# Performance work log

Hardware: AMD Instinct MI355X
Metric: run time of the kernel (lower is better)

## Reference

```python
import jax, jax.numpy as jnp
import numpy as np

BN_EPS = 1e-5
R = 8.0        # radius
L = 11         # sequence kernel size (odd), s = L//2
K = 24         # kernel_channels[-1]
N_NODES = 32768
N_EDGES = 524288
C_IN = 128     # in_channels == out_channels
C_W = 32       # width = out_channels * base_width / 64


def _bn(x, gamma, beta):
    # BatchNorm1d in training mode: biased batch statistics over node dim
    mu = jnp.mean(x, axis=0)
    var = jnp.mean(jnp.square(x - mu), axis=0)
    return (x - mu) * jax.lax.rsqrt(var + BN_EPS) * gamma + beta


def _lrelu(x, slope):
    return jnp.where(x >= 0, x, slope * x)


def setup_inputs() -> dict:
    key = jax.random.key(0)
    ks = jax.random.split(key, 10)

    def glorot(k, shape, fan_in):
        return jax.random.normal(k, shape, jnp.float32) * np.float32(1.0 / np.sqrt(fan_in))

    inp = {}
    inp["x"] = jax.random.normal(ks[0], (N_NODES, C_IN), jnp.float32)
    inp["pos"] = jax.random.normal(ks[1], (N_NODES, 3), jnp.float32) * 10.0
    inp["ori"] = jax.random.normal(ks[2], (N_NODES, 9), jnp.float32)
    inp["seq"] = jnp.arange(N_NODES, dtype=jnp.int32)
    inp["edge_index"] = jax.random.randint(ks[3], (2, N_EDGES), 0, N_NODES, jnp.int32)
    # input MLP params: BN(C_IN) -> LeakyReLU(0.1) -> Linear(C_IN->C_W, no bias) -> BN(C_W) -> LeakyReLU(0.1)
    inp["bn1_g"] = jnp.ones((C_IN,), jnp.float32)
    inp["bn1_b"] = jnp.zeros((C_IN,), jnp.float32)
    inp["lin1_w"] = glorot(ks[4], (C_IN, C_W), C_IN)
    inp["bn2_g"] = jnp.ones((C_W,), jnp.float32)
    inp["bn2_b"] = jnp.zeros((C_W,), jnp.float32)
    # CDConv WeightNet (single layer kernel_channels=[K]): per-seq-bin affine 7 -> K
    inp["wn_w"] = glorot(ks[5], (L, 7, K), 7)
    inp["wn_b"] = jnp.zeros((L, K), jnp.float32)
    # CDConv output projection: [K*C_W, C_W]
    inp["conv_w"] = glorot(ks[6], (K * C_W, C_W), K * C_W)
    # output Linear: BN(C_W) -> LeakyReLU(0.1) -> Linear(C_W->C_IN, no bias)
    inp["bn3_g"] = jnp.ones((C_W,), jnp.float32)
    inp["bn3_b"] = jnp.zeros((C_W,), jnp.float32)
    inp["lin2_w"] = glorot(ks[7], (C_W, C_IN), C_W)
    return inp


def reference(x, pos, ori, seq, edge_index,
              bn1_g, bn1_b, lin1_w, bn2_g, bn2_b,
              wn_w, wn_b, conv_w, bn3_g, bn3_b, lin2_w):
    n = x.shape[0]
    identity = x  # in_channels == out_channels -> identity branch is passthrough

    # ----- input MLP (mid_channels=None) -----
    h = _lrelu(_bn(x, bn1_g, bn1_b), 0.1)
    h = h @ lin1_w                       # [N, C_W]
    h = _lrelu(_bn(h, bn2_g, bn2_b), 0.1)

    # ----- CDConv: continuous geometric kernel over neighbor edges -----
    src, dst = edge_index[0], edge_index[1]      # message j=src -> i=dst
    d = pos[src] - pos[dst]                      # [E,3]
    dist = jnp.linalg.norm(d, axis=-1, keepdims=True)
    direction = d / (dist + 1e-9)
    Ri = ori[dst].reshape(-1, 3, 3)              # receiver local frame
    Rj = ori[src].reshape(-1, 3, 3)
    pos_local = jnp.einsum('eij,ej->ei', Ri, direction)      # direction in local frame
    ori_feat = jnp.einsum('eij,ej->ei', Ri, Rj[:, 0, :])     # neighbor axis in local frame
    delta = jnp.concatenate([pos_local, ori_feat, dist / R], axis=-1)  # [E,7]

    s = L // 2
    sidx = jnp.clip(seq[src] - seq[dst], -s, s) + s          # [E] in [0, L)

    # WeightNet: per-edge affine selected by sequence bin, LeakyReLU(0.2)
    w = _lrelu(jnp.einsum('ef,efk->ek', delta, wn_w[sidx]) + wn_b[sidx], 0.2)  # [E,K]

    # message = outer(kernel_weight, x_j), scatter-sum to receivers
    msg = (w[:, :, None] * h[src][:, None, :]).reshape(w.shape[0], K * C_W)   # [E, K*C_W]
    agg = jax.ops.segment_sum(msg, dst, num_segments=n)                        # [N, K*C_W]
    h = agg @ conv_w                                                            # [N, C_W]

    # ----- output Linear + residual -----
    h = _lrelu(_bn(h, bn3_g, bn3_b), 0.1)
    out = h @ lin2_w + identity
    return out
```

## Files before the change

kernel.cpp:

```cpp
#include <hip/hip_runtime.h>

#define N_NODES 32768
#define C_IN 128
#define C_W 32
#define KK 24
#define SS 5
#define GG 8

__global__ void __launch_bounds__(256) k_pre(
        const float* __restrict__ x, float* __restrict__ s1,
        const int* __restrict__ ei, int E, int* __restrict__ counts) {
    int t = threadIdx.x;
    int c = t % C_IN;
    int r0 = blockIdx.x * 2 + t / C_IN;
    float s = 0.f, sq = 0.f;
    for (int r = r0; r < N_NODES; r += 512) {
        float v = x[(size_t)r * C_IN + c];
        s += v; sq += v * v;
    }
    atomicAdd(&s1[c], s);
    atomicAdd(&s1[C_IN + c], sq);
    for (int e = blockIdx.x * 256 + t; e < E; e += 256 * 256)
        atomicAdd(&counts[ei[E + e]], 1);
}

__global__ void __launch_bounds__(256) k_mlp1(
        const float* __restrict__ x, const float* __restrict__ s1,
        const float* __restrict__ g1, const float* __restrict__ b1,
        const float* __restrict__ w1, float* __restrict__ hpre,
        float* __restrict__ s2sh) {
    __shared__ float sAB[2][C_IN];
    __shared__ float sx[32][C_IN + 4];
    __shared__ float sw[C_IN][C_W];
    const int t = threadIdx.x;
    const int row0 = blockIdx.x * 32;
    if (t < C_IN) {
        float mean = s1[t] * (1.f / N_NODES);
        float var = s1[C_IN + t] * (1.f / N_NODES) - mean * mean;
        float a = g1[t] * rsqrtf(var + 1e-5f);
        sAB[0][t] = a; sAB[1][t] = b1[t] - mean * a;
    }
    for (int idx = t; idx < C_IN * C_W; idx += 256)
        sw[idx / C_W][idx % C_W] = w1[idx];
    __syncthreads();
    for (int idx = t; idx < 32 * 32; idx += 256) {
        int r = idx >> 5, cq = idx & 31;
        float4 v = *(const float4*)&x[(size_t)(row0 + r) * C_IN + cq * 4];
        float* d = &sx[r][cq * 4];
        float a0 = sAB[0][cq*4+0]*v.x + sAB[1][cq*4+0];
        float a1 = sAB[0][cq*4+1]*v.y + sAB[1][cq*4+1];
        float a2 = sAB[0][cq*4+2]*v.z + sAB[1][cq*4+2];
        float a3 = sAB[0][cq*4+3]*v.w + sAB[1][cq*4+3];
        d[0] = a0 >= 0.f ? a0 : 0.1f * a0;
        d[1] = a1 >= 0.f ? a1 : 0.1f * a1;
        d[2] = a2 >= 0.f ? a2 : 0.1f * a2;
        d[3] = a3 >= 0.f ? a3 : 0.1f * a3;
    }
    __syncthreads();
    const int r = t >> 3, c0 = (t & 7) * 4;
    float ac0 = 0.f, ac1 = 0.f, ac2 = 0.f, ac3 = 0.f;
    #pragma unroll 8
    for (int cc = 0; cc < C_IN; ++cc) {
        float xv = sx[r][cc];
        float4 wv = *(const float4*)&sw[cc][c0];
        ac0 += xv * wv.x; ac1 += xv * wv.y; ac2 += xv * wv.z; ac3 += xv * wv.w;
    }
    float4 o; o.x = ac0; o.y = ac1; o.z = ac2; o.w = ac3;
    *(float4*)&hpre[(size_t)(row0 + r) * C_W + c0] = o;
    __syncthreads();
    sx[r][c0] = ac0; sx[r][c0+1] = ac1; sx[r][c0+2] = ac2; sx[r][c0+3] = ac3;
    __syncthreads();
    if (t < C_W) {
        float s = 0.f, sq = 0.f;
        #pragma unroll
        for (int rr = 0; rr < 32; ++rr) {
            float v = sx[rr][t];
            s += v; sq += v * v;
        }
        int sh = (blockIdx.x & 7) * 64;
        atomicAdd(&s2sh[sh + t], s);
        atomicAdd(&s2sh[sh + C_W + t], sq);
    }
}

__global__ void __launch_bounds__(1024) k_scan1(
        const int* __restrict__ counts, int* __restrict__ scanned,
        int* __restrict__ blockSums) {
    __shared__ int s[1024];
    int t = threadIdx.x;
    int i = blockIdx.x * 1024 + t;
    int v = counts[i];
    s[t] = v;
    __syncthreads();
    for (int d = 1; d < 1024; d <<= 1) {
        int u = (t >= d) ? s[t - d] : 0;
        __syncthreads();
        s[t] += u;
        __syncthreads();
    }
    scanned[i] = s[t] - v;
    if (t == 1023) blockSums[blockIdx.x] = s[1023];
}

__global__ void k_scan2(int* __restrict__ blockSums, int* __restrict__ blockOff,
                        int* __restrict__ offsets) {
    __shared__ int s[32];
    int t = threadIdx.x;
    int v = blockSums[t];
    s[t] = v;
    __syncthreads();
    for (int d = 1; d < 32; d <<= 1) {
        int u = (t >= d) ? s[t - d] : 0;
        __syncthreads();
        s[t] += u;
        __syncthreads();
    }
    blockOff[t] = s[t] - v;
    if (t == 31) offsets[N_NODES] = s[31];
}

__global__ void __launch_bounds__(1024) k_scan3(
        const int* __restrict__ scanned, const int* __restrict__ blockOff,
        int* __restrict__ offsets, int* __restrict__ cursor) {
    int t = threadIdx.x;
    int i = blockIdx.x * 1024 + t;
    int v = scanned[i] + blockOff[blockIdx.x];
    offsets[i] = v;
    cursor[i] = v;
}

__global__ void __launch_bounds__(256) k_edge(
        const int* __restrict__ ei, int E,
        const float* __restrict__ pos, const float* __restrict__ ori,
        const int* __restrict__ seq,
        const float* __restrict__ wnw, const float* __restrict__ wnb,
        int* __restrict__ cursor, int* __restrict__ srcPerm,
        float* __restrict__ wPerm) {
    __shared__ float sWnw[11][169];
    __shared__ float sWnb[11][24];
    const int t = threadIdx.x;
    for (int idx = t; idx < 11 * 168; idx += 256)
        sWnw[idx / 168][idx % 168] = wnw[idx];
    for (int idx = t; idx < 11 * 24; idx += 256)
        sWnb[idx / 24][idx % 24] = wnb[idx];
    __syncthreads();
    const int e = blockIdx.x * 256 + t;
    if (e >= E) return;
    const int src = ei[e];
    const int dst = ei[E + e];
    int ds = seq[src] - seq[dst];
    ds = ds < -SS ? -SS : (ds > SS ? SS : ds);
    const int sb = ds + SS;
    float dx = pos[src * 3 + 0] - pos[dst * 3 + 0];
    float dy = pos[src * 3 + 1] - pos[dst * 3 + 1];
    float dz = pos[src * 3 + 2] - pos[dst * 3 + 2];
    float dist = sqrtf(dx * dx + dy * dy + dz * dz);
    float inv = 1.f / (dist + 1e-9f);
    float ux = dx * inv, uy = dy * inv, uz = dz * inv;
    float b0 = ori[src * 9 + 0], b1 = ori[src * 9 + 1], b2 = ori[src * 9 + 2];
    float delta[7];
    #pragma unroll
    for (int r = 0; r < 3; ++r) {
        float m0 = ori[dst * 9 + r * 3 + 0];
        float m1 = ori[dst * 9 + r * 3 + 1];
        float m2 = ori[dst * 9 + r * 3 + 2];
        delta[r]     = m0 * ux + m1 * uy + m2 * uz;
        delta[3 + r] = m0 * b0 + m1 * b1 + m2 * b2;
    }
    delta[6] = dist * 0.125f;
    float w[KK];
    #pragma unroll
    for (int k = 0; k < KK; ++k) {
        float acc = sWnb[sb][k];
        #pragma unroll
        for (int f = 0; f < 7; ++f)
            acc += delta[f] * sWnw[sb][f * 24 + k];
        w[k] = acc >= 0.f ? acc : 0.2f * acc;
    }
    const int p = atomicAdd(&cursor[dst], 1);
    srcPerm[p] = src;
    float4* wp = (float4*)(wPerm + (size_t)p * KK);
    #pragma unroll
    for (int q = 0; q < 6; ++q) {
        float4 o; o.x = w[q*4]; o.y = w[q*4+1]; o.z = w[q*4+2]; o.w = w[q*4+3];
        wp[q] = o;
    }
}

__global__ void __launch_bounds__(256) k_node(
    const int* __restrict__ offsets, const int* __restrict__ srcPerm,
    const float* __restrict__ wPerm, const float* __restrict__ hpre,
    const float* __restrict__ s2sh, const float* __restrict__ g2,
    const float* __restrict__ b2, const float* __restrict__ convw,
    float* __restrict__ convout, float* __restrict__ s3sh) {
    __shared__ float sA2[C_W], sB2[C_W];
    __shared__ int sOff[GG + 1];
    __shared__ float sAgg[GG][KK * C_W];
    __shared__ float sRv[GG][C_W], sRq[GG][C_W];
    const int i0 = blockIdx.x * GG;
    const int t = threadIdx.x;
    if (t < C_W) {
        float s = 0.f, sq = 0.f;
        #pragma unroll
        for (int j = 0; j < 8; ++j) {
            s  += s2sh[j * 64 + t];
            sq += s2sh[j * 64 + C_W + t];
        }
        float mean = s * (1.f / N_NODES);
        float var = sq * (1.f / N_NODES) - mean * mean;
        float a = g2[t] * rsqrtf(var + 1e-5f);
        sA2[t] = a; sB2[t] = b2[t] - mean * a;
    }
    if (t <= GG) sOff[t] = offsets[i0 + t];
    __syncthreads();
    const int g = t >> 5, c = t & 31;
    const float bnA = sA2[c], bnB = sB2[c];
    int p = sOff[g];
    const int pEnd = sOff[g + 1];
    float a[KK];
    #pragma unroll
    for (int k = 0; k < KK; ++k) a[k] = 0.f;

    int srcCur = (p < pEnd) ? srcPerm[p] : 0;
    for (; p < pEnd; ++p) {
        int srcNxt = (p + 1 < pEnd) ? srcPerm[p + 1] : 0;
        float hr = hpre[(size_t)srcCur * C_W + c];
        const float4* wr = (const float4*)(wPerm + (size_t)p * KK);
        float4 w0 = wr[0], w1 = wr[1], w2 = wr[2];
        float4 w3 = wr[3], w4 = wr[4], w5 = wr[5];
        float v = bnA * hr + bnB;
        v = v >= 0.f ? v : 0.1f * v;
        a[0]  += w0.x * v; a[1]  += w0.y * v; a[2]  += w0.z * v; a[3]  += w0.w * v;
        a[4]  += w1.x * v; a[5]  += w1.y * v; a[6]  += w1.z * v; a[7]  += w1.w * v;
        a[8]  += w2.x * v; a[9]  += w2.y * v; a[10] += w2.z * v; a[11] += w2.w * v;
        a[12] += w3.x * v; a[13] += w3.y * v; a[14] += w3.z * v; a[15] += w3.w * v;
        a[16] += w4.x * v; a[17] += w4.y * v; a[18] += w4.z * v; a[19] += w4.w * v;
        a[20] += w5.x * v; a[21] += w5.y * v; a[22] += w5.z * v; a[23] += w5.w * v;
        srcCur = srcNxt;
    }
    #pragma unroll
    for (int k = 0; k < KK; ++k) sAgg[g][k * C_W + c] = a[k];
    __syncthreads();
    float p0 = 0.f, p1 = 0.f;
    for (int r = 0; r < KK * C_W; r += 8) {
        float4 v0 = *(const float4*)&sAgg[g][r];
        float4 v1 = *(const float4*)&sAgg[g][r + 4];
        p0 += v0.x * convw[(r + 0) * 32 + c] + v0.y * convw[(r + 1) * 32 + c]
            + v0.z * convw[(r + 2) * 32 + c] + v0.w * convw[(r + 3) * 32 + c];
        p1 += v1.x * convw[(r + 4) * 32 + c] + v1.y * convw[(r + 5) * 32 + c]
            + v1.z * convw[(r + 6) * 32 + c] + v1.w * convw[(r + 7) * 32 + c];
    }
    float v = p0 + p1;
    convout[(size_t)(i0 + g) * C_W + c] = v;
    sRv[g][c] = v; sRq[g][c] = v * v;
    __syncthreads();
    if (t < 64) {
        int cc = t & 31;
        bool isq = t >= C_W;
        float s = 0.f;
        #pragma unroll
        for (int gg = 0; gg < GG; ++gg)
            s += isq ? sRq[gg][cc] : sRv[gg][cc];
        atomicAdd(&s3sh[(blockIdx.x & 7) * 64 + t], s);
    }
}

__global__ void __launch_bounds__(256) k_out(
        const float* __restrict__ conv, const float* __restrict__ s3sh,
        const float* __restrict__ g3, const float* __restrict__ b3,
        const float* __restrict__ w2, const float* __restrict__ x,
        float* __restrict__ out) {
    __shared__ float sAB[2][C_W];
    __shared__ float sh[8][C_W];
    __shared__ float sw2[C_W][C_IN];
    const int t = threadIdx.x;
    const int row0 = blockIdx.x * 8;
    if (t < C_W) {
        float s = 0.f, sq = 0.f;
        #pragma unroll
        for (int j = 0; j < 8; ++j) {
            s  += s3sh[j * 64 + t];
            sq += s3sh[j * 64 + C_W + t];
        }
        float mean = s * (1.f / N_NODES);
        float var = sq * (1.f / N_NODES) - mean * mean;
        float a = g3[t] * rsqrtf(var + 1e-5f);
        sAB[0][t] = a; sAB[1][t] = b3[t] - mean * a;
    }
    for (int idx = t; idx < C_W * C_IN; idx += 256)
        sw2[idx >> 7][idx & 127] = w2[idx];
    __syncthreads();
    {
        float v = conv[(size_t)row0 * C_W + t];
        int r = t >> 5, cc = t & 31;
        v = sAB[0][cc] * v + sAB[1][cc];
        sh[r][cc] = v >= 0.f ? v : 0.1f * v;
    }
    __syncthreads();
    const int c = t & 127, rq = t >> 7;
    float acc[4];
    #pragma unroll
    for (int j = 0; j < 4; ++j)
        acc[j] = x[(size_t)(row0 + rq + j * 2) * C_IN + c];
    #pragma unroll 4
    for (int cw = 0; cw < C_W; ++cw) {
        float wv = sw2[cw][c];
        #pragma unroll
        for (int j = 0; j < 4; ++j)
            acc[j] += sh[rq + j * 2][cw] * wv;
    }
    #pragma unroll
    for (int j = 0; j < 4; ++j)
        out[(size_t)(row0 + rq + j * 2) * C_IN + c] = acc[j];
}

extern "C" void kernel_launch(void* const* d_in, const int* in_sizes, int n_in,
                              void* d_out, int out_size, void* d_ws, size_t ws_size,
                              hipStream_t stream) {
    const float* x     = (const float*)d_in[0];
    const float* pos   = (const float*)d_in[1];
    const float* ori   = (const float*)d_in[2];
    const int*   seq   = (const int*)d_in[3];
    const int*   ei    = (const int*)d_in[4];
    const float* bn1g  = (const float*)d_in[5];
    const float* bn1b  = (const float*)d_in[6];
    const float* lin1w = (const float*)d_in[7];
    const float* bn2g  = (const float*)d_in[8];
    const float* bn2b  = (const float*)d_in[9];
    const float* wnw   = (const float*)d_in[10];
    const float* wnb   = (const float*)d_in[11];
    const float* convw = (const float*)d_in[12];
    const float* bn3g  = (const float*)d_in[13];
    const float* bn3b  = (const float*)d_in[14];
    const float* lin2w = (const float*)d_in[15];
    float* out = (float*)d_out;
    const int E = in_sizes[4] / 2;

    char* wsb = (char*)d_ws;
    size_t off = 0;
    auto alloc = [&](size_t bytes) {
        void* p = wsb + off;
        off = (off + bytes + 255) & ~(size_t)255;
        return p;
    };
    float* s1      = (float*)alloc(256 * 4);
    float* s2sh    = (float*)alloc(512 * 4);
    float* s3sh    = (float*)alloc(512 * 4);
    int*   counts  = (int*)alloc((size_t)N_NODES * 4);
    size_t zero_bytes = off;
    int*   scanned = (int*)alloc((size_t)N_NODES * 4);
    int*   bsums   = (int*)alloc(64 * 4);
    int*   boff    = (int*)alloc(64 * 4);
    int*   offsets = (int*)alloc(((size_t)N_NODES + 1) * 4);
    int*   cursor  = (int*)alloc((size_t)N_NODES * 4);
    int*   srcPerm = (int*)alloc((size_t)E * 4);
    float* hpre    = (float*)alloc((size_t)N_NODES * C_W * 4);
    float* convo   = (float*)alloc((size_t)N_NODES * C_W * 4);
    float* wPerm   = (float*)alloc((size_t)E * KK * 4);

    hipMemsetAsync(wsb, 0, zero_bytes, stream);

    k_pre<<<256, 256, 0, stream>>>(x, s1, ei, E, counts);
    k_mlp1<<<N_NODES / 32, 256, 0, stream>>>(x, s1, bn1g, bn1b, lin1w, hpre, s2sh);
    k_scan1<<<32, 1024, 0, stream>>>(counts, scanned, bsums);
    k_scan2<<<1, 32, 0, stream>>>(bsums, boff, offsets);
    k_scan3<<<32, 1024, 0, stream>>>(scanned, boff, offsets, cursor);
    k_edge<<<(E + 255) / 256, 256, 0, stream>>>(ei, E, pos, ori, seq, wnw, wnb,
                                                cursor, srcPerm, wPerm);
    k_node<<<N_NODES / GG, 256, 0, stream>>>(offsets, srcPerm, wPerm, hpre,
                                             s2sh, bn2g, bn2b, convw, convo, s3sh);
    k_out<<<N_NODES / 8, 256, 0, stream>>>(convo, s3sh, bn3g, bn3b, lin2w, x, out);
}
```

Baseline: 290.1 us.

## Merge scans into one kernel, batch neighbor gathers, vectorize output projection

Replaces the three-kernel prefix scan with a single 1024-thread block in which each thread scans 32 counts serially before a block-wide scan, removing two launches and the intermediate buffers. The k_node gather loop now loads 32 source indices cooperatively, broadcasts them with shuffles and unrolls four edges at a time so more hpre and weight loads are in flight. The k_out projection is changed to float4 loads and stores per thread. k_mlp1 is moved after k_edge, and the unrolled node loop raises register pressure.

```diff
diff --git a/kernel.cpp b/kernel.cpp
--- a/kernel.cpp
+++ b/kernel.cpp
@@ -6,6 +6,17 @@
 #define KK 24
 #define SS 5
 #define GG 8
+
+#define LD6(W, PTR) do { const float4* _p = (const float4*)(PTR); \
+  W[0]=_p[0]; W[1]=_p[1]; W[2]=_p[2]; W[3]=_p[3]; W[4]=_p[4]; W[5]=_p[5]; } while(0)
+
+#define ACC24(W, V) do { float _v = (V); \
+  a[0]+=W[0].x*_v;  a[1]+=W[0].y*_v;  a[2]+=W[0].z*_v;  a[3]+=W[0].w*_v;  \
+  a[4]+=W[1].x*_v;  a[5]+=W[1].y*_v;  a[6]+=W[1].z*_v;  a[7]+=W[1].w*_v;  \
+  a[8]+=W[2].x*_v;  a[9]+=W[2].y*_v;  a[10]+=W[2].z*_v; a[11]+=W[2].w*_v; \
+  a[12]+=W[3].x*_v; a[13]+=W[3].y*_v; a[14]+=W[3].z*_v; a[15]+=W[3].w*_v; \
+  a[16]+=W[4].x*_v; a[17]+=W[4].y*_v; a[18]+=W[4].z*_v; a[19]+=W[4].w*_v; \
+  a[20]+=W[5].x*_v; a[21]+=W[5].y*_v; a[22]+=W[5].z*_v; a[23]+=W[5].w*_v; } while(0)
 
 __global__ void __launch_bounds__(256) k_pre(
         const float* __restrict__ x, float* __restrict__ s1,
@@ -83,50 +94,43 @@
     }
 }
 
-__global__ void __launch_bounds__(1024) k_scan1(
-        const int* __restrict__ counts, int* __restrict__ scanned,
-        int* __restrict__ blockSums) {
-    __shared__ int s[1024];
-    int t = threadIdx.x;
-    int i = blockIdx.x * 1024 + t;
-    int v = counts[i];
-    s[t] = v;
+__global__ void __launch_bounds__(1024) k_scan(
+        const int* __restrict__ counts, int* __restrict__ offsets,
+        int* __restrict__ cursor) {
+    __shared__ int sblk[1024];
+    const int t = threadIdx.x;
+    const int base = t * 32;
+    const int4* cp = (const int4*)(counts + base);
+    int loc[32];
+    int s = 0;
+    #pragma unroll
+    for (int q = 0; q < 8; ++q) {
+        int4 v = cp[q];
+        loc[q*4+0] = s; s += v.x;
+        loc[q*4+1] = s; s += v.y;
+        loc[q*4+2] = s; s += v.z;
+        loc[q*4+3] = s; s += v.w;
+    }
+    sblk[t] = s;
     __syncthreads();
     for (int d = 1; d < 1024; d <<= 1) {
-        int u = (t >= d) ? s[t - d] : 0;
+        int u = (t >= d) ? sblk[t - d] : 0;
         __syncthreads();
-        s[t] += u;
+        sblk[t] += u;
         __syncthreads();
     }
-    scanned[i] = s[t] - v;
-    if (t == 1023) blockSums[blockIdx.x] = s[1023];
-}
-
-__global__ void k_scan2(int* __restrict__ blockSums, int* __restrict__ blockOff,
-                        int* __restrict__ offsets) {
-    __shared__ int s[32];
-    int t = threadIdx.x;
-    int v = blockSums[t];
-    s[t] = v;
-    __syncthreads();
-    for (int d = 1; d < 32; d <<= 1) {
-        int u = (t >= d) ? s[t - d] : 0;
-        __syncthreads();
-        s[t] += u;
-        __syncthreads();
-    }
-    blockOff[t] = s[t] - v;
-    if (t == 31) offsets[N_NODES] = s[31];
-}
-
-__global__ void __launch_bounds__(1024) k_scan3(
-        const int* __restrict__ scanned, const int* __restrict__ blockOff,
-        int* __restrict__ offsets, int* __restrict__ cursor) {
-    int t = threadIdx.x;
-    int i = blockIdx.x * 1024 + t;
-    int v = scanned[i] + blockOff[blockIdx.x];
-    offsets[i] = v;
-    cursor[i] = v;
+    const int blockbase = sblk[t] - s;
+    #pragma unroll
+    for (int q = 0; q < 8; ++q) {
+        int4 o;
+        o.x = blockbase + loc[q*4+0];
+        o.y = blockbase + loc[q*4+1];
+        o.z = blockbase + loc[q*4+2];
+        o.w = blockbase + loc[q*4+3];
+        ((int4*)(offsets + base))[q] = o;
+        ((int4*)(cursor + base))[q] = o;
+    }
+    if (t == 1023) offsets[N_NODES] = sblk[1023];
 }
 
 __global__ void __launch_bounds__(256) k_edge(
@@ -215,28 +219,47 @@
     __syncthreads();
     const int g = t >> 5, c = t & 31;
     const float bnA = sA2[c], bnB = sB2[c];
-    int p = sOff[g];
-    const int pEnd = sOff[g + 1];
+    const int beg = sOff[g], end = sOff[g + 1];
     float a[KK];
     #pragma unroll
     for (int k = 0; k < KK; ++k) a[k] = 0.f;
 
-    int srcCur = (p < pEnd) ? srcPerm[p] : 0;
-    for (; p < pEnd; ++p) {
-        int srcNxt = (p + 1 < pEnd) ? srcPerm[p + 1] : 0;
-        float hr = hpre[(size_t)srcCur * C_W + c];
-        const float4* wr = (const float4*)(wPerm + (size_t)p * KK);
-        float4 w0 = wr[0], w1 = wr[1], w2 = wr[2];
-        float4 w3 = wr[3], w4 = wr[4], w5 = wr[5];
-        float v = bnA * hr + bnB;
-        v = v >= 0.f ? v : 0.1f * v;
-        a[0]  += w0.x * v; a[1]  += w0.y * v; a[2]  += w0.z * v; a[3]  += w0.w * v;
-        a[4]  += w1.x * v; a[5]  += w1.y * v; a[6]  += w1.z * v; a[7]  += w1.w * v;
-        a[8]  += w2.x * v; a[9]  += w2.y * v; a[10] += w2.z * v; a[11] += w2.w * v;
-        a[12] += w3.x * v; a[13] += w3.y * v; a[14] += w3.z * v; a[15] += w3.w * v;
-        a[16] += w4.x * v; a[17] += w4.y * v; a[18] += w4.z * v; a[19] += w4.w * v;
-        a[20] += w5.x * v; a[21] += w5.y * v; a[22] += w5.z * v; a[23] += w5.w * v;
-        srcCur = srcNxt;
+    for (int cb = beg; cb < end; cb += 32) {
+        const int m = min(32, end - cb);
+        int srcL = (cb + c < end) ? srcPerm[cb + c] : 0;
+        int j = 0;
+        for (; j + 4 <= m; j += 4) {
+            int s0 = __shfl(srcL, j + 0, 32);
+            int s1 = __shfl(srcL, j + 1, 32);
+            int s2 = __shfl(srcL, j + 2, 32);
+            int s3 = __shfl(srcL, j + 3, 32);
+            float h0 = hpre[(size_t)s0 * C_W + c];
+            float h1 = hpre[(size_t)s1 * C_W + c];
+            float h2 = hpre[(size_t)s2 * C_W + c];
+            float h3 = hpre[(size_t)s3 * C_W + c];
+            float4 wa[6], wb[6], wc[6], wd[6];
+            const float* wbase = wPerm + (size_t)(cb + j) * KK;
+            LD6(wa, wbase);
+            LD6(wb, wbase + KK);
+            LD6(wc, wbase + 2 * KK);
+            LD6(wd, wbase + 3 * KK);
+            float v0 = bnA * h0 + bnB; v0 = v0 >= 0.f ? v0 : 0.1f * v0;
+            float v1 = bnA * h1 + bnB; v1 = v1 >= 0.f ? v1 : 0.1f * v1;
+            float v2 = bnA * h2 + bnB; v2 = v2 >= 0.f ? v2 : 0.1f * v2;
+            float v3 = bnA * h3 + bnB; v3 = v3 >= 0.f ? v3 : 0.1f * v3;
+            ACC24(wa, v0);
+            ACC24(wb, v1);
+            ACC24(wc, v2);
+            ACC24(wd, v3);
+        }
+        for (; j < m; ++j) {
+            int s0 = __shfl(srcL, j, 32);
+            float h0 = hpre[(size_t)s0 * C_W + c];
+            float4 wa[6];
+            LD6(wa, wPerm + (size_t)(cb + j) * KK);
+            float v0 = bnA * h0 + bnB; v0 = v0 >= 0.f ? v0 : 0.1f * v0;
+            ACC24(wa, v0);
+        }
     }
     #pragma unroll
     for (int k = 0; k < KK; ++k) sAgg[g][k * C_W + c] = a[k];
@@ -297,21 +320,16 @@
         sh[r][cc] = v >= 0.f ? v : 0.1f * v;
     }
     __syncthreads();
-    const int c = t & 127, rq = t >> 7;
-    float acc[4];
-    #pragma unroll
-    for (int j = 0; j < 4; ++j)
-        acc[j] = x[(size_t)(row0 + rq + j * 2) * C_IN + c];
-    #pragma unroll 4
+    const int r = t >> 5, c4 = (t & 31) * 4;
+    float4 acc = *(const float4*)&x[(size_t)(row0 + r) * C_IN + c4];
+    #pragma unroll 8
     for (int cw = 0; cw < C_W; ++cw) {
-        float wv = sw2[cw][c];
-        #pragma unroll
-        for (int j = 0; j < 4; ++j)
-            acc[j] += sh[rq + j * 2][cw] * wv;
-    }
-    #pragma unroll
-    for (int j = 0; j < 4; ++j)
-        out[(size_t)(row0 + rq + j * 2) * C_IN + c] = acc[j];
+        float hv = sh[r][cw];
+        float4 wv = *(const float4*)&sw2[cw][c4];
+        acc.x += hv * wv.x; acc.y += hv * wv.y;
+        acc.z += hv * wv.z; acc.w += hv * wv.w;
+    }
+    *(float4*)&out[(size_t)(row0 + r) * C_IN + c4] = acc;
 }
 
 extern "C" void kernel_launch(void* const* d_in, const int* in_sizes, int n_in,
@@ -348,9 +366,6 @@
     float* s3sh    = (float*)alloc(512 * 4);
     int*   counts  = (int*)alloc((size_t)N_NODES * 4);
     size_t zero_bytes = off;
-    int*   scanned = (int*)alloc((size_t)N_NODES * 4);
-    int*   bsums   = (int*)alloc(64 * 4);
-    int*   boff    = (int*)alloc(64 * 4);
     int*   offsets = (int*)alloc(((size_t)N_NODES + 1) * 4);
     int*   cursor  = (int*)alloc((size_t)N_NODES * 4);
     int*   srcPerm = (int*)alloc((size_t)E * 4);
@@ -361,12 +376,10 @@
     hipMemsetAsync(wsb, 0, zero_bytes, stream);
 
     k_pre<<<256, 256, 0, stream>>>(x, s1, ei, E, counts);
-    k_mlp1<<<N_NODES / 32, 256, 0, stream>>>(x, s1, bn1g, bn1b, lin1w, hpre, s2sh);
-    k_scan1<<<32, 1024, 0, stream>>>(counts, scanned, bsums);
-    k_scan2<<<1, 32, 0, stream>>>(bsums, boff, offsets);
-    k_scan3<<<32, 1024, 0, stream>>>(scanned, boff, offsets, cursor);
+    k_scan<<<1, 1024, 0, stream>>>(counts, offsets, cursor);
     k_edge<<<(E + 255) / 256, 256, 0, stream>>>(ei, E, pos, ori, seq, wnw, wnb,
                                                 cursor, srcPerm, wPerm);
+    k_mlp1<<<N_NODES / 32, 256, 0, stream>>>(x, s1, bn1g, bn1b, lin1w, hpre, s2sh);
     k_node<<<N_NODES / GG, 256, 0, stream>>>(offsets, srcPerm, wPerm, hpre,
                                              s2sh, bn2g, bn2b, convw, convo, s3sh);
     k_out<<<N_NODES / 8, 256, 0, stream>>>(convo, s3sh, bn3g, bn3b, lin2w, x, out);
```

Measured after the change: 286.0 us. About the same (-1.4%).
